# Kernel optimization log

Measured on AMD Instinct MI355X. Metric: run time of the kernel, lower is better.

The kernel has to match this reference:

```python
import jax, jax.numpy as jnp
import numpy as np

N_NODES = 100000
N_EDGES = 1600000
IN_DIM = 64
OUT_DIM = 64
HIDDEN = 64  # fixed in edge_weight_mlp
POS_DIM = 3


def setup_inputs() -> dict:
    key = jax.random.key(0)
    ks = jax.random.split(key, 10)
    x = jax.random.normal(ks[0], (N_NODES, IN_DIM), dtype=jnp.float32)
    edge_index = jax.random.randint(ks[1], (2, N_EDGES), 0, N_NODES, dtype=jnp.int64)
    pos = jax.random.normal(ks[2], (N_NODES, POS_DIM), dtype=jnp.float32)
    # edge_weight_mlp params: Linear(2*IN_DIM+1 -> 64), Linear(64 -> 1)
    s1 = 1.0 / np.sqrt(2 * IN_DIM + 1)
    w1 = jax.random.uniform(ks[3], (2 * IN_DIM + 1, HIDDEN), jnp.float32, -s1, s1)
    b1 = jax.random.uniform(ks[4], (HIDDEN,), jnp.float32, -s1, s1)
    s2 = 1.0 / np.sqrt(HIDDEN)
    w2 = jax.random.uniform(ks[5], (HIDDEN, 1), jnp.float32, -s2, s2)
    b2 = jax.random.uniform(ks[6], (1,), jnp.float32, -s2, s2)
    # transform: Linear(IN_DIM -> OUT_DIM)
    st = 1.0 / np.sqrt(IN_DIM)
    wt = jax.random.uniform(ks[7], (IN_DIM, OUT_DIM), jnp.float32, -st, st)
    bt = jax.random.uniform(ks[8], (OUT_DIM,), jnp.float32, -st, st)
    return {"x": x, "edge_index": edge_index, "pos": pos,
            "w1": w1, "b1": b1, "w2": w2, "b2": b2, "wt": wt, "bt": bt}


def reference(x, edge_index, pos, w1, b1, w2, b2, wt, bt):
    src, dst = edge_index[0], edge_index[1]
    # edge weights: MLP on [x_src, x_dst, |pos_dst - pos_src|]
    edge_length = jnp.linalg.norm(pos[dst] - pos[src], axis=1, keepdims=True)  # [E,1]
    edge_feat = jnp.concatenate([x[src], x[dst], edge_length], axis=1)  # [E, 2*in+1]
    h = jax.nn.relu(edge_feat @ w1 + b1)
    edge_weights = jax.nn.sigmoid(h @ w2 + b2)  # [E,1]
    # node transform, gather, weight, scatter-add
    x_t = x @ wt + bt  # [N, out]
    messages = x_t[src] * edge_weights  # [E, out]
    out = jax.ops.segment_sum(messages, dst, num_segments=x.shape[0])  # [N, out]
    return out, edge_weights
```

## Files before the change

### kernel.cpp

```cpp
#include <hip/hip_runtime.h>
#include <hip/hip_bf16.h>
#include <math.h>

#define NN 100000
#define NE 1600000
#define CAP 48
#define NB 391
#define BCAP 4608
#define EPB 4096
#define NBLKA ((NE + EPB - 1) / EPB)
#define PSTR 72

typedef __attribute__((ext_vector_type(8))) short short8;
typedef __attribute__((ext_vector_type(4))) float floatx4;

static __device__ __forceinline__ unsigned short f2bb(float f) {
    __hip_bfloat16 h = __float2bfloat16(f);
    return *(unsigned short*)&h;
}

__global__ __launch_bounds__(256) void prep_mfma(
    const float* __restrict__ x, const float* __restrict__ w1,
    const float* __restrict__ b1,
    unsigned int* __restrict__ rec, unsigned short* __restrict__ hd) {
    __shared__ unsigned short As[64 * PSTR];
    __shared__ unsigned short Bs[128 * PSTR];
    int t = threadIdx.x;
    int nbase = blockIdx.x * 64;
    {
        int r = t & 63;
        int node = nbase + r; if (node >= NN) node = NN - 1;
        const float4* xr = (const float4*)(x + (size_t)node * 64);
#pragma unroll
        for (int i = 0; i < 4; ++i) {
            int s = (t >> 6) + 4 * i;
            float4 v = xr[s];
            ushort4 o = {f2bb(v.x), f2bb(v.y), f2bb(v.z), f2bb(v.w)};
            *(ushort4*)&As[r * PSTR + s * 4] = o;
        }
    }
    {
        int n = t & 127;
        int kh = t >> 7;
        int krow = (n < 64) ? 0 : 64;
        int col = n & 63;
#pragma unroll
        for (int i = 0; i < 32; ++i) {
            int k = kh * 32 + i;
            Bs[n * PSTR + k] = f2bb(w1[(krow + k) * 64 + col]);
        }
    }
    __syncthreads();
    int lane = t & 63, wave = t >> 6;
    int grp = lane >> 4, l15 = lane & 15;
    floatx4 acc[8] = {};
    int arow = wave * 16 + l15;
#pragma unroll
    for (int ks = 0; ks < 2; ++ks) {
        int koff = ks * 32 + grp * 8;
        short8 a = *(const short8*)&As[arow * PSTR + koff];
#pragma unroll
        for (int nt = 0; nt < 8; ++nt) {
            short8 b = *(const short8*)&Bs[(nt * 16 + l15) * PSTR + koff];
            acc[nt] = __builtin_amdgcn_mfma_f32_16x16x32_bf16(a, b, acc[nt], 0, 0, 0);
        }
    }
#pragma unroll
    for (int nt = 0; nt < 8; ++nt) {
#pragma unroll
        for (int r = 0; r < 4; ++r) {
            int nr = wave * 16 + grp * 4 + r;
            int node = nbase + nr;
            if (node >= NN) continue;
            if (nt < 4) {
                int col = nt * 16 + l15;
                unsigned xbits = As[nr * PSTR + col];
                rec[(size_t)node * 64 + col] =
                    ((unsigned)f2bb(acc[nt][r]) << 16) | xbits;
            } else {
                int col = (nt - 4) * 16 + l15;
                hd[(size_t)node * 64 + col] = f2bb(acc[nt][r] + b1[col]);
            }
        }
    }
}

__global__ __launch_bounds__(256) void bucket_kernel(
    const int* __restrict__ ei, int* __restrict__ gcursor,
    uint2* __restrict__ bucketed) {
    __shared__ int cnt[NB];
    __shared__ int base_s[NB];
    int t = threadIdx.x;
    for (int i = t; i < NB; i += 256) cnt[i] = 0;
    __syncthreads();
    int e0 = blockIdx.x * EPB;
    unsigned int tags[16];
#pragma unroll
    for (int i = 0; i < 16; ++i) {
        int e = e0 + i * 256 + t;
        tags[i] = 0xFFFFFFFFu;
        if (e < NE) {
            int dst = ei[NE + e];
            int b = dst >> 8;
            int slot = atomicAdd(&cnt[b], 1);
            tags[i] = ((unsigned)b << 12) | (unsigned)slot;
        }
    }
    __syncthreads();
    for (int b = t; b < NB; b += 256)
        base_s[b] = atomicAdd(&gcursor[b], cnt[b]);
    __syncthreads();
#pragma unroll
    for (int i = 0; i < 16; ++i) {
        if (tags[i] != 0xFFFFFFFFu) {
            int e = e0 + i * 256 + t;
            int b = (int)(tags[i] >> 12);
            int slot = (int)(tags[i] & 0xFFFu);
            int pos = base_s[b] + slot;
            if (pos < BCAP) {
                unsigned src = (unsigned)ei[e];
                unsigned dst = (unsigned)ei[NE + e];
                bucketed[(size_t)b * BCAP + pos] =
                    make_uint2(src | ((dst & 255u) << 17), (unsigned)e);
            }
        }
    }
}

__global__ __launch_bounds__(1024) void csr_kernel(
    const uint2* __restrict__ bucketed, const int* __restrict__ gcursor,
    uint2* __restrict__ pairs, int* __restrict__ deg) {
    __shared__ int cur[256];
    int t = threadIdx.x;
    if (t < 256) cur[t] = 0;
    __syncthreads();
    int b = blockIdx.x;
    int n0 = b << 8;
    int cnt = gcursor[b];
    if (cnt > BCAP) cnt = BCAP;
    for (int i = t; i < cnt; i += 1024) {
        uint2 en = bucketed[(size_t)b * BCAP + i];
        int dwb = (int)((en.x >> 17) & 255u);
        unsigned src = en.x & 0x1FFFFu;
        int slot = atomicAdd(&cur[dwb], 1);
        if (slot < CAP)
            pairs[(size_t)(n0 + dwb) * CAP + slot] = make_uint2(src, en.y);
    }
    __syncthreads();
    if (t < 256) {
        int node = n0 + t;
        if (node < NN) deg[node] = (cur[t] > CAP) ? CAP : cur[t];
    }
}

__global__ __launch_bounds__(256) void mega_kernel(
    const uint2* __restrict__ pairs, const int* __restrict__ deg,
    const unsigned int* __restrict__ rec, const unsigned short* __restrict__ hd,
    const float* __restrict__ pos, const float* __restrict__ w1,
    const float* __restrict__ w2, const float* __restrict__ b2,
    float* __restrict__ ew_out, unsigned short* __restrict__ aggb,
    float* __restrict__ sumw) {
    int t = threadIdx.x;
    int w = t >> 6, lane = t & 63;
    int e4 = lane >> 4, hg = lane & 15;
    int node = blockIdx.x * 4 + w;
    if (node >= NN) return;

    float acc0 = 0.f, acc1 = 0.f, acc2 = 0.f, acc3 = 0.f, sw = 0.f;
    int d = deg[node];
    uint2 hz = ((const uint2*)(hd + (size_t)node * 64))[hg];
    float zb0 = __uint_as_float(hz.x << 16);
    float zb1 = __uint_as_float(hz.x & 0xFFFF0000u);
    float zb2 = __uint_as_float(hz.y << 16);
    float zb3 = __uint_as_float(hz.y & 0xFFFF0000u);
    float4 w24 = ((const float4*)w2)[hg];
    float4 wl4 = ((const float4*)(w1 + 128 * 64))[hg];
    float pdx = pos[node * 3 + 0], pdy = pos[node * 3 + 1], pdz = pos[node * 3 + 2];
    float b2v = b2[0];
    const uint2* seg = pairs + (size_t)node * CAP;

    for (int j = 0; j < d; j += 4) {
        int idx = j + e4;
        if (idx > d - 1) idx = d - 1;
        bool valid = (j + e4 < d);
        uint2 pr = seg[idx];
        int src = (int)pr.x;
        uint4 u4 = ((const uint4*)rec)[(size_t)src * 16 + hg];

        float dx = pdx - pos[src * 3 + 0];
        float dy = pdy - pos[src * 3 + 1];
        float dz = pdz - pos[src * 3 + 2];
        float len = __builtin_amdgcn_sqrtf(dx * dx + dy * dy + dz * dz);

        float z0 = zb0 + __uint_as_float(u4.x & 0xFFFF0000u) + len * wl4.x;
        float z1 = zb1 + __uint_as_float(u4.y & 0xFFFF0000u) + len * wl4.y;
        float z2 = zb2 + __uint_as_float(u4.z & 0xFFFF0000u) + len * wl4.z;
        float z3 = zb3 + __uint_as_float(u4.w & 0xFFFF0000u) + len * wl4.w;
        float tt = fmaxf(z0, 0.f) * w24.x;
        tt = fmaf(fmaxf(z1, 0.f), w24.y, tt);
        tt = fmaf(fmaxf(z2, 0.f), w24.z, tt);
        tt = fmaf(fmaxf(z3, 0.f), w24.w, tt);
        tt += __shfl_xor(tt, 1);
        tt += __shfl_xor(tt, 2);
        tt += __shfl_xor(tt, 4);
        tt += __shfl_xor(tt, 8);
        float ew = __builtin_amdgcn_rcpf(1.f + __expf(-(tt + b2v)));
        if (valid) {
            if (hg == 0) ew_out[pr.y] = ew;
            acc0 = fmaf(ew, __uint_as_float(u4.x << 16), acc0);
            acc1 = fmaf(ew, __uint_as_float(u4.y << 16), acc1);
            acc2 = fmaf(ew, __uint_as_float(u4.z << 16), acc2);
            acc3 = fmaf(ew, __uint_as_float(u4.w << 16), acc3);
            sw += ew;
        }
    }
#pragma unroll
    for (int off = 16; off < 64; off <<= 1) {
        acc0 += __shfl_xor(acc0, off);
        acc1 += __shfl_xor(acc1, off);
        acc2 += __shfl_xor(acc2, off);
        acc3 += __shfl_xor(acc3, off);
        sw   += __shfl_xor(sw, off);
    }
    if (e4 == 0) {
        ushort4 o = {f2bb(acc0), f2bb(acc1), f2bb(acc2), f2bb(acc3)};
        *(ushort4*)(aggb + (size_t)node * 64 + hg * 4) = o;
    }
    if (lane == 0) sumw[node] = sw;
}

__global__ __launch_bounds__(256) void transform_mfma(
    const unsigned short* __restrict__ aggb, const float* __restrict__ sumw,
    const float* __restrict__ wt, const float* __restrict__ bt,
    float* __restrict__ out) {
    __shared__ unsigned short As[64 * PSTR];
    __shared__ unsigned short Bs[64 * PSTR];
    int t = threadIdx.x;
    int nbase = blockIdx.x * 64;
    {
        int r = t & 63;
        int node = nbase + r; if (node >= NN) node = NN - 1;
        const uint4* ar = (const uint4*)(aggb + (size_t)node * 64);
#pragma unroll
        for (int i = 0; i < 2; ++i) {
            int s = (t >> 6) + 4 * i;
            *(uint4*)&As[r * PSTR + s * 8] = ar[s];
        }
    }
    {
        int n = t & 63;
        int kq = t >> 6;
#pragma unroll
        for (int i = 0; i < 16; ++i) {
            int k = kq * 16 + i;
            Bs[n * PSTR + k] = f2bb(wt[k * 64 + n]);
        }
    }
    __syncthreads();
    int lane = t & 63, wave = t >> 6;
    int grp = lane >> 4, l15 = lane & 15;
    floatx4 acc[4] = {};
    int arow = wave * 16 + l15;
#pragma unroll
    for (int ks = 0; ks < 2; ++ks) {
        int koff = ks * 32 + grp * 8;
        short8 a = *(const short8*)&As[arow * PSTR + koff];
#pragma unroll
        for (int nt = 0; nt < 4; ++nt) {
            short8 b = *(const short8*)&Bs[(nt * 16 + l15) * PSTR + koff];
            acc[nt] = __builtin_amdgcn_mfma_f32_16x16x32_bf16(a, b, acc[nt], 0, 0, 0);
        }
    }
#pragma unroll
    for (int nt = 0; nt < 4; ++nt) {
        int col = nt * 16 + l15;
        float btv = bt[col];
#pragma unroll
        for (int r = 0; r < 4; ++r) {
            int node = nbase + wave * 16 + grp * 4 + r;
            if (node < NN)
                out[(size_t)node * 64 + col] = acc[nt][r] + sumw[node] * btv;
        }
    }
}

extern "C" void kernel_launch(void* const* d_in, const int* in_sizes, int n_in,
                              void* d_out, int out_size, void* d_ws, size_t ws_size,
                              hipStream_t stream) {
    const float* x   = (const float*)d_in[0];
    const int*   ei  = (const int*)d_in[1];
    const float* pos = (const float*)d_in[2];
    const float* w1  = (const float*)d_in[3];
    const float* b1  = (const float*)d_in[4];
    const float* w2  = (const float*)d_in[5];
    const float* b2  = (const float*)d_in[6];
    const float* wt  = (const float*)d_in[7];
    const float* bt  = (const float*)d_in[8];

    float* out    = (float*)d_out;
    float* ew_out = out + (size_t)NN * 64;

    unsigned int* rec = (unsigned int*)d_ws;
    unsigned short* hd = (unsigned short*)(rec + (size_t)NN * 64);
    uint2* pairs = (uint2*)(hd + (size_t)NN * 64);
    unsigned short* aggb = (unsigned short*)(pairs + (size_t)NN * CAP);
    float* sumw = (float*)(aggb + (size_t)NN * 64);
    int* gcursor = (int*)(sumw + NN);
    int* deg = gcursor + NB;

    uint2* bucketed = (uint2*)d_out;

    hipMemsetAsync(gcursor, 0, NB * sizeof(int), stream);
    prep_mfma<<<(NN + 63) / 64, 256, 0, stream>>>(x, w1, b1, rec, hd);
    bucket_kernel<<<NBLKA, 256, 0, stream>>>(ei, gcursor, bucketed);
    csr_kernel<<<NB, 1024, 0, stream>>>(bucketed, gcursor, pairs, deg);
    mega_kernel<<<(NN + 3) / 4, 256, 0, stream>>>(pairs, deg, rec, hd, pos,
                                                  w1, w2, b2, ew_out, aggb, sumw);
    transform_mfma<<<(NN + 63) / 64, 256, 0, stream>>>(aggb, sumw, wt, bt, out);
}
```

Measured before the change: 277.8 us.

## Software-pipeline edge gathers in mega kernel and pad positions to float4

The per-node edge loop in mega_kernel now prefetches the next group's pair index, source record and source position while computing the current group, so dependent gather latency can overlap with arithmetic. Positions are repacked into a padded float4 array during prep, so each source position becomes one 16-byte load instead of three scalar loads. The bucket kernel keeps src/dst values in registers instead of rereading edge_index in its second pass. The trade-off is more registers for the prefetch state and extra workspace for the padded position array.

```diff
diff --git a/kernel.cpp b/kernel.cpp
--- a/kernel.cpp
+++ b/kernel.cpp
@@ -21,8 +21,9 @@
 
 __global__ __launch_bounds__(256) void prep_mfma(
     const float* __restrict__ x, const float* __restrict__ w1,
-    const float* __restrict__ b1,
-    unsigned int* __restrict__ rec, unsigned short* __restrict__ hd) {
+    const float* __restrict__ b1, const float* __restrict__ pos,
+    unsigned int* __restrict__ rec, unsigned short* __restrict__ hd,
+    float4* __restrict__ pos4) {
     __shared__ unsigned short As[64 * PSTR];
     __shared__ unsigned short Bs[128 * PSTR];
     int t = threadIdx.x;
@@ -49,6 +50,12 @@
             int k = kh * 32 + i;
             Bs[n * PSTR + k] = f2bb(w1[(krow + k) * 64 + col]);
         }
+    }
+    if (t < 64) {
+        int node = nbase + t;
+        if (node < NN)
+            pos4[node] = make_float4(pos[node * 3 + 0], pos[node * 3 + 1],
+                                     pos[node * 3 + 2], 0.f);
     }
     __syncthreads();
     int lane = t & 63, wave = t >> 6;
@@ -95,13 +102,15 @@
     __syncthreads();
     int e0 = blockIdx.x * EPB;
     unsigned int tags[16];
+    int srcs[16], dsts[16];
 #pragma unroll
     for (int i = 0; i < 16; ++i) {
         int e = e0 + i * 256 + t;
         tags[i] = 0xFFFFFFFFu;
         if (e < NE) {
-            int dst = ei[NE + e];
-            int b = dst >> 8;
+            srcs[i] = ei[e];
+            dsts[i] = ei[NE + e];
+            int b = dsts[i] >> 8;
             int slot = atomicAdd(&cnt[b], 1);
             tags[i] = ((unsigned)b << 12) | (unsigned)slot;
         }
@@ -118,10 +127,9 @@
             int slot = (int)(tags[i] & 0xFFFu);
             int pos = base_s[b] + slot;
             if (pos < BCAP) {
-                unsigned src = (unsigned)ei[e];
-                unsigned dst = (unsigned)ei[NE + e];
                 bucketed[(size_t)b * BCAP + pos] =
-                    make_uint2(src | ((dst & 255u) << 17), (unsigned)e);
+                    make_uint2((unsigned)srcs[i] | (((unsigned)dsts[i] & 255u) << 17),
+                               (unsigned)e);
             }
         }
     }
@@ -156,7 +164,7 @@
 __global__ __launch_bounds__(256) void mega_kernel(
     const uint2* __restrict__ pairs, const int* __restrict__ deg,
     const unsigned int* __restrict__ rec, const unsigned short* __restrict__ hd,
-    const float* __restrict__ pos, const float* __restrict__ w1,
+    const float4* __restrict__ pos4, const float* __restrict__ w1,
     const float* __restrict__ w2, const float* __restrict__ b2,
     float* __restrict__ ew_out, unsigned short* __restrict__ aggb,
     float* __restrict__ sumw) {
@@ -175,43 +183,57 @@
     float zb3 = __uint_as_float(hz.y & 0xFFFF0000u);
     float4 w24 = ((const float4*)w2)[hg];
     float4 wl4 = ((const float4*)(w1 + 128 * 64))[hg];
-    float pdx = pos[node * 3 + 0], pdy = pos[node * 3 + 1], pdz = pos[node * 3 + 2];
+    float4 pd = pos4[node];
     float b2v = b2[0];
     const uint2* seg = pairs + (size_t)node * CAP;
 
-    for (int j = 0; j < d; j += 4) {
-        int idx = j + e4;
-        if (idx > d - 1) idx = d - 1;
-        bool valid = (j + e4 < d);
-        uint2 pr = seg[idx];
-        int src = (int)pr.x;
-        uint4 u4 = ((const uint4*)rec)[(size_t)src * 16 + hg];
-
-        float dx = pdx - pos[src * 3 + 0];
-        float dy = pdy - pos[src * 3 + 1];
-        float dz = pdz - pos[src * 3 + 2];
-        float len = __builtin_amdgcn_sqrtf(dx * dx + dy * dy + dz * dz);
-
-        float z0 = zb0 + __uint_as_float(u4.x & 0xFFFF0000u) + len * wl4.x;
-        float z1 = zb1 + __uint_as_float(u4.y & 0xFFFF0000u) + len * wl4.y;
-        float z2 = zb2 + __uint_as_float(u4.z & 0xFFFF0000u) + len * wl4.z;
-        float z3 = zb3 + __uint_as_float(u4.w & 0xFFFF0000u) + len * wl4.w;
-        float tt = fmaxf(z0, 0.f) * w24.x;
-        tt = fmaf(fmaxf(z1, 0.f), w24.y, tt);
-        tt = fmaf(fmaxf(z2, 0.f), w24.z, tt);
-        tt = fmaf(fmaxf(z3, 0.f), w24.w, tt);
-        tt += __shfl_xor(tt, 1);
-        tt += __shfl_xor(tt, 2);
-        tt += __shfl_xor(tt, 4);
-        tt += __shfl_xor(tt, 8);
-        float ew = __builtin_amdgcn_rcpf(1.f + __expf(-(tt + b2v)));
-        if (valid) {
-            if (hg == 0) ew_out[pr.y] = ew;
-            acc0 = fmaf(ew, __uint_as_float(u4.x << 16), acc0);
-            acc1 = fmaf(ew, __uint_as_float(u4.y << 16), acc1);
-            acc2 = fmaf(ew, __uint_as_float(u4.z << 16), acc2);
-            acc3 = fmaf(ew, __uint_as_float(u4.w << 16), acc3);
-            sw += ew;
+    if (d > 0) {
+        int i0 = (e4 < d) ? e4 : (d - 1);
+        uint2 pr_c = seg[i0];
+        int i1 = (4 + e4 < d) ? (4 + e4) : (d - 1);
+        uint2 pr_n = (4 < d) ? seg[i1] : pr_c;
+        uint4 u_c = ((const uint4*)rec)[(size_t)pr_c.x * 16 + hg];
+        float4 ps_c = pos4[pr_c.x];
+
+        for (int j = 0; j < d; j += 4) {
+            int jn = j + 4;
+            uint2 pr_n2 = pr_n;
+            uint4 u_n = u_c;
+            float4 ps_n = ps_c;
+            if (jn < d) {
+                u_n = ((const uint4*)rec)[(size_t)pr_n.x * 16 + hg];
+                ps_n = pos4[pr_n.x];
+                int i2 = (jn + 4 + e4 < d) ? (jn + 4 + e4) : (d - 1);
+                if (jn + 4 < d) pr_n2 = seg[i2];
+            }
+            bool valid = (j + e4 < d);
+            float dx = pd.x - ps_c.x;
+            float dy = pd.y - ps_c.y;
+            float dz = pd.z - ps_c.z;
+            float len = __builtin_amdgcn_sqrtf(dx * dx + dy * dy + dz * dz);
+
+            float z0 = zb0 + __uint_as_float(u_c.x & 0xFFFF0000u) + len * wl4.x;
+            float z1 = zb1 + __uint_as_float(u_c.y & 0xFFFF0000u) + len * wl4.y;
+            float z2 = zb2 + __uint_as_float(u_c.z & 0xFFFF0000u) + len * wl4.z;
+            float z3 = zb3 + __uint_as_float(u_c.w & 0xFFFF0000u) + len * wl4.w;
+            float tt = fmaxf(z0, 0.f) * w24.x;
+            tt = fmaf(fmaxf(z1, 0.f), w24.y, tt);
+            tt = fmaf(fmaxf(z2, 0.f), w24.z, tt);
+            tt = fmaf(fmaxf(z3, 0.f), w24.w, tt);
+            tt += __shfl_xor(tt, 1);
+            tt += __shfl_xor(tt, 2);
+            tt += __shfl_xor(tt, 4);
+            tt += __shfl_xor(tt, 8);
+            float ew = __builtin_amdgcn_rcpf(1.f + __expf(-(tt + b2v)));
+            if (valid) {
+                if (hg == 0) ew_out[pr_c.y] = ew;
+                acc0 = fmaf(ew, __uint_as_float(u_c.x << 16), acc0);
+                acc1 = fmaf(ew, __uint_as_float(u_c.y << 16), acc1);
+                acc2 = fmaf(ew, __uint_as_float(u_c.z << 16), acc2);
+                acc3 = fmaf(ew, __uint_as_float(u_c.w << 16), acc3);
+                sw += ew;
+            }
+            pr_c = pr_n; pr_n = pr_n2; u_c = u_n; ps_c = ps_n;
         }
     }
 #pragma unroll
@@ -304,17 +326,18 @@
     unsigned short* hd = (unsigned short*)(rec + (size_t)NN * 64);
     uint2* pairs = (uint2*)(hd + (size_t)NN * 64);
     unsigned short* aggb = (unsigned short*)(pairs + (size_t)NN * CAP);
-    float* sumw = (float*)(aggb + (size_t)NN * 64);
+    float4* pos4 = (float4*)(aggb + (size_t)NN * 64);
+    float* sumw = (float*)(pos4 + NN);
     int* gcursor = (int*)(sumw + NN);
     int* deg = gcursor + NB;
 
     uint2* bucketed = (uint2*)d_out;
 
     hipMemsetAsync(gcursor, 0, NB * sizeof(int), stream);
-    prep_mfma<<<(NN + 63) / 64, 256, 0, stream>>>(x, w1, b1, rec, hd);
+    prep_mfma<<<(NN + 63) / 64, 256, 0, stream>>>(x, w1, b1, pos, rec, hd, pos4);
     bucket_kernel<<<NBLKA, 256, 0, stream>>>(ei, gcursor, bucketed);
     csr_kernel<<<NB, 1024, 0, stream>>>(bucketed, gcursor, pairs, deg);
-    mega_kernel<<<(NN + 3) / 4, 256, 0, stream>>>(pairs, deg, rec, hd, pos,
+    mega_kernel<<<(NN + 3) / 4, 256, 0, stream>>>(pairs, deg, rec, hd, pos4,
                                                   w1, w2, b2, ew_out, aggb, sumw);
     transform_mfma<<<(NN + 63) / 64, 256, 0, stream>>>(aggb, sumw, wt, bt, out);
 }
```

New measurement: 259.3 us. 6.7% less time.
